# Performance work log

Hardware: AMD Instinct MI355X
Metric: run time of the kernel (lower is better)

## Reference

```python
import jax, jax.numpy as jnp
import numpy as np

L, B, D, N_LAYERS = 2048, 32, 1024, 4


def setup_inputs() -> dict:
    key = jax.random.key(0)
    ks = jax.random.split(key, 5)
    # PyTorch Linear default init: U(-1/sqrt(fan_in), 1/sqrt(fan_in))
    bound = 1.0 / np.sqrt(D)
    x = jax.random.normal(ks[0], (L, B, D), dtype=jnp.float32)
    A_log = jnp.log(0.99) * jnp.ones((D,), dtype=jnp.float32)  # matches torch init
    layers_W = jax.random.uniform(ks[1], (N_LAYERS, D, D), jnp.float32, -bound, bound)
    layers_b = jax.random.uniform(ks[2], (N_LAYERS, D), jnp.float32, -bound, bound)
    head_W = jax.random.uniform(ks[3], (1, D), jnp.float32, -bound, bound)
    head_b = jax.random.uniform(ks[4], (1,), jnp.float32, -bound, bound)
    return {"x": x, "A_log": A_log, "layers_W": layers_W, "layers_b": layers_b,
            "head_W": head_W, "head_b": head_b}


def reference(x, A_log, layers_W, layers_b, head_W, head_b):
    Lx, Bx, Dx = x.shape
    # log_P[t] = (t+1) * A_log  (cumsum of the constant log_A along time)
    log_P = jnp.cumsum(jnp.broadcast_to(A_log[None, None, :], (Lx, Bx, Dx)), axis=0)
    P = jnp.exp(log_P)                       # [L, B, D]
    h = P * jnp.cumsum(x / P, axis=0)        # diagonal linear SSM scan
    for i in range(layers_W.shape[0]):
        h = jnp.tanh(jnp.einsum('lbd,ed->lbe', h, layers_W[i]) + layers_b[i])
    out = jnp.einsum('lbd,ed->lbe', h, head_W) + head_b  # [L, B, 1]
    return out.squeeze(-1)                   # [L, B]
```

## Files before the change

kernel.cpp:

```cpp
#include <hip/hip_runtime.h>
#include <cstdint>
#include <cstddef>

#define LSEQ 2048
#define BB   32
#define DD   1024
#define NLAYERS 4
#define MM   (LSEQ*BB)
#define BD   (BB*DD)
#define CHUNK 32
#define NCHUNK (LSEQ/CHUNK)

typedef _Float16 f16;
typedef __attribute__((ext_vector_type(8))) _Float16 f16x8;
typedef __attribute__((ext_vector_type(4))) float f32x4;


__global__ void scan_pass1(const float* __restrict__ x, const float* __restrict__ Alog,
                           f16* __restrict__ h, float* __restrict__ carry) {
    int tid = blockIdx.x * blockDim.x + threadIdx.x;
    int bd  = tid & (BD - 1);
    int c   = tid >> 15;
    float a = expf(Alog[bd & (DD - 1)]);
    size_t base = (size_t)c * CHUNK * BD + bd;
    float hv = 0.f;
#pragma unroll
    for (int i = 0; i < CHUNK; ++i) {
        hv = a * hv + x[base + (size_t)i * BD];
        h[base + (size_t)i * BD] = (f16)hv;
    }
    carry[c * BD + bd] = hv;
}

__global__ void scan_pass2(const float* __restrict__ Alog, float* __restrict__ carry) {
    int bd = blockIdx.x * blockDim.x + threadIdx.x;
    float d32 = expf((float)CHUNK * Alog[bd & (DD - 1)]);
    float cin = 0.f;
    for (int c = 0; c < NCHUNK; ++c) {
        float co = carry[c * BD + bd];
        carry[c * BD + bd] = cin;
        cin = d32 * cin + co;
    }
}

__global__ void scan_pass3(const float* __restrict__ Alog, const float* __restrict__ carry,
                           f16* __restrict__ h) {
    int tid = blockIdx.x * blockDim.x + threadIdx.x;
    int bd  = tid & (BD - 1);
    int c   = tid >> 15;
    float a   = expf(Alog[bd & (DD - 1)]);
    float cin = carry[c * BD + bd];
    size_t base = (size_t)c * CHUNK * BD + bd;
    float p = a;
#pragma unroll
    for (int i = 0; i < CHUNK; ++i) {
        size_t idx = base + (size_t)i * BD;
        float hv = (float)h[idx] + p * cin;
        h[idx] = (f16)hv;
        p *= a;
    }
}


__global__ void cvt_w(const float* __restrict__ w, f16* __restrict__ o, int n) {
    int i = (blockIdx.x * blockDim.x + threadIdx.x) * 4;
    if (i + 3 < n) {
        float4 v = *(const float4*)&w[i];
        o[i + 0] = (f16)v.x; o[i + 1] = (f16)v.y;
        o[i + 2] = (f16)v.z; o[i + 3] = (f16)v.w;
    }
}


#define BM 256
#define BN 256
#define BK 64
#define KK 1024
#define NN 1024
#define NKTILE (KK / BK)
#define NITER  (NKTILE / 2)

__device__ __forceinline__ void gload_lds16(const void* g, void* l) {
    __builtin_amdgcn_global_load_lds((const __attribute__((address_space(1))) unsigned int*)g,
                                     (__attribute__((address_space(3))) unsigned int*)l,
                                     16, 0, 0);
}

__device__ __forceinline__ void stage_half(const f16* __restrict__ gbase, f16* region, int tid) {
#pragma unroll
    for (int j = 0; j < 2; ++j) {
        int s = tid + j * 512;
        int r = s >> 3;
        int c = (s & 7) ^ (r & 7);
        gload_lds16(gbase + (size_t)r * KK + c * 8, region + (size_t)s * 8);
    }
}

__device__ __forceinline__ void stage_tile(const f16* __restrict__ gA, const f16* __restrict__ gW,
                                           f16* As, f16* Bs, int tid) {
    stage_half(gA,                    As,        tid);
    stage_half(gA + (size_t)128 * KK, As + 8192, tid);
    stage_half(gW,                    Bs,        tid);
    stage_half(gW + (size_t)128 * KK, Bs + 8192, tid);
}

__device__ __forceinline__ f16x8 rd(const f16* base, int row, int chunk) {
    int c = chunk ^ (row & 7);
    return *(const f16x8*)(base + row * 64 + c * 8);
}

__device__ __forceinline__ float tanh_fast(float z) {
    float e = __expf(2.f * z);
    return 1.f - 2.f / (e + 1.f);
}

#define BAR() do { __builtin_amdgcn_sched_barrier(0); __builtin_amdgcn_s_barrier(); \
                   __builtin_amdgcn_sched_barrier(0); } while (0)

__global__ __launch_bounds__(512, 2) void gemm_tanh(const f16* __restrict__ A,
                                                    const f16* __restrict__ W,
                                                    const float* __restrict__ bias,
                                                    f16* __restrict__ C) {
    __shared__ f16 As[2][BM * BK];
    __shared__ f16 Bs[2][BN * BK];

    const int tid  = threadIdx.x;
    const int lane = tid & 63;
    const int wid  = tid >> 6;
    const int wr   = wid >> 2;
    const int wc   = wid & 3;

    const int cpx = gridDim.x >> 3;
    const int lin = ((int)blockIdx.x & 7) * cpx + ((int)blockIdx.x >> 3);
    const int tm  = (lin >> 2) * BM;
    const int tn  = (lin & 3) * BN;

    const f16* Ab = A + (size_t)tm * KK;
    const f16* Wb = W + (size_t)tn * KK;

    const int fr = lane & 15;
    const int fc = lane >> 4;

    f32x4 acc[8][4];
#pragma unroll
    for (int i = 0; i < 8; ++i)
#pragma unroll
        for (int j = 0; j < 4; ++j)
            acc[i][j] = (f32x4){0.f, 0.f, 0.f, 0.f};

    stage_tile(Ab,      Wb,      &As[0][0], &Bs[0][0], tid);
    stage_tile(Ab + 64, Wb + 64, &As[1][0], &Bs[1][0], tid);
    asm volatile("s_waitcnt vmcnt(8)" ::: "memory");
    BAR();

    const int arow = wr * 128 + fr;
    const int brow = wc * 64  + fr;

    for (int it = 0; it < NITER; ++it) {
        const bool pf = (it + 1 < NITER);
        const int kt0 = 2 * it;
        const f16* Ac = &As[0][0]; const f16* Bc = &Bs[0][0];
        const f16* Ad = &As[1][0]; const f16* Bd = &Bs[1][0];
        f16x8 a0[8], b0[4], a1[8], b1[4];

#pragma unroll
        for (int m = 0; m < 8; ++m) a0[m] = rd(Ac, arow + m * 16, fc);
#pragma unroll
        for (int n = 0; n < 4; ++n) b0[n] = rd(Bc, brow + n * 16, fc);
#pragma unroll
        for (int m = 0; m < 8; ++m) a1[m] = rd(Ac, arow + m * 16, 4 + fc);
#pragma unroll
        for (int n = 0; n < 4; ++n) b1[n] = rd(Bc, brow + n * 16, 4 + fc);
        BAR();
        __builtin_amdgcn_s_setprio(1);
#pragma unroll
        for (int m = 0; m < 8; ++m)
#pragma unroll
            for (int n = 0; n < 4; ++n)
                acc[m][n] = __builtin_amdgcn_mfma_f32_16x16x32_f16(a0[m], b0[n], acc[m][n], 0, 0, 0);
        __builtin_amdgcn_s_setprio(0);
        asm volatile("s_waitcnt lgkmcnt(0)" ::: "memory");
        BAR();

        if (pf) stage_tile(Ab + (size_t)(kt0 + 2) * BK, Wb + (size_t)(kt0 + 2) * BK,
                           &As[0][0], &Bs[0][0], tid);
        __builtin_amdgcn_s_setprio(1);
#pragma unroll
        for (int m = 0; m < 8; ++m)
#pragma unroll
            for (int n = 0; n < 4; ++n)
                acc[m][n] = __builtin_amdgcn_mfma_f32_16x16x32_f16(a1[m], b1[n], acc[m][n], 0, 0, 0);
        __builtin_amdgcn_s_setprio(0);
        if (pf) asm volatile("s_waitcnt vmcnt(8)" ::: "memory");
        else    asm volatile("s_waitcnt vmcnt(0)" ::: "memory");
        BAR();

#pragma unroll
        for (int m = 0; m < 8; ++m) a0[m] = rd(Ad, arow + m * 16, fc);
#pragma unroll
        for (int n = 0; n < 4; ++n) b0[n] = rd(Bd, brow + n * 16, fc);
#pragma unroll
        for (int m = 0; m < 8; ++m) a1[m] = rd(Ad, arow + m * 16, 4 + fc);
#pragma unroll
        for (int n = 0; n < 4; ++n) b1[n] = rd(Bd, brow + n * 16, 4 + fc);
        BAR();
        __builtin_amdgcn_s_setprio(1);
#pragma unroll
        for (int m = 0; m < 8; ++m)
#pragma unroll
            for (int n = 0; n < 4; ++n)
                acc[m][n] = __builtin_amdgcn_mfma_f32_16x16x32_f16(a0[m], b0[n], acc[m][n], 0, 0, 0);
        __builtin_amdgcn_s_setprio(0);
        asm volatile("s_waitcnt lgkmcnt(0)" ::: "memory");
        BAR();

        if (pf) stage_tile(Ab + (size_t)(kt0 + 3) * BK, Wb + (size_t)(kt0 + 3) * BK,
                           &As[1][0], &Bs[1][0], tid);
        __builtin_amdgcn_s_setprio(1);
#pragma unroll
        for (int m = 0; m < 8; ++m)
#pragma unroll
            for (int n = 0; n < 4; ++n)
                acc[m][n] = __builtin_amdgcn_mfma_f32_16x16x32_f16(a1[m], b1[n], acc[m][n], 0, 0, 0);
        __builtin_amdgcn_s_setprio(0);
        if (pf) asm volatile("s_waitcnt vmcnt(8)" ::: "memory");
        else    asm volatile("s_waitcnt vmcnt(0)" ::: "memory");
        BAR();
    }

#pragma unroll
    for (int mi = 0; mi < 8; ++mi) {
        const int r0 = tm + wr * 128 + mi * 16 + (fc << 2);
#pragma unroll
        for (int ni = 0; ni < 4; ++ni) {
            const int c = tn + wc * 64 + ni * 16 + fr;
            const float bv = bias[c];
#pragma unroll
            for (int q = 0; q < 4; ++q) {
                float z = acc[mi][ni][q] + bv;
                C[(size_t)(r0 + q) * NN + c] = (f16)tanh_fast(z);
            }
        }
    }
}


__global__ void head_k(const f16* __restrict__ h, const float* __restrict__ hw,
                       const float* __restrict__ hb, float* __restrict__ out) {
    const int row  = blockIdx.x * 4 + (threadIdx.x >> 6);
    const int lane = threadIdx.x & 63;
    const f16* hr = h + (size_t)row * DD;
    float s = 0.f;
#pragma unroll
    for (int j = 0; j < DD / 64; ++j) {
        int d = lane + j * 64;
        s += (float)hr[d] * hw[d];
    }
#pragma unroll
    for (int o = 32; o > 0; o >>= 1) s += __shfl_down(s, o, 64);
    if (lane == 0) out[row] = s + hb[0];
}


extern "C" void kernel_launch(void* const* d_in, const int* in_sizes, int n_in,
                              void* d_out, int out_size, void* d_ws, size_t ws_size,
                              hipStream_t stream) {
    const float* x    = (const float*)d_in[0];
    const float* Alog = (const float*)d_in[1];
    const float* Wls  = (const float*)d_in[2];
    const float* bls  = (const float*)d_in[3];
    const float* hw   = (const float*)d_in[4];
    const float* hb   = (const float*)d_in[5];
    float* out = (float*)d_out;

    char* ws = (char*)d_ws;
    const size_t hbytes = (size_t)MM * DD * sizeof(f16);
    f16* h0 = (f16*)ws;
    f16* h1 = (f16*)(ws + hbytes);
    char* scratch = ws + 2 * hbytes;
    float* carry = (float*)scratch;
    f16*   wf    = (f16*)scratch;

    scan_pass1<<<(NCHUNK * BD) / 256, 256, 0, stream>>>(x, Alog, h0, carry);
    scan_pass2<<<BD / 256, 256, 0, stream>>>(Alog, carry);
    scan_pass3<<<(NCHUNK * BD) / 256, 256, 0, stream>>>(Alog, carry, h0);

    cvt_w<<<(NLAYERS * DD * DD / 4) / 256, 256, 0, stream>>>(Wls, wf, NLAYERS * DD * DD);

    dim3 grid((MM / BM) * (NN / BN)), blk(512);
    gemm_tanh<<<grid, blk, 0, stream>>>(h0, wf + 0 * (DD * DD), bls + 0 * DD, h1);
    gemm_tanh<<<grid, blk, 0, stream>>>(h1, wf + 1 * (DD * DD), bls + 1 * DD, h0);
    gemm_tanh<<<grid, blk, 0, stream>>>(h0, wf + 2 * (DD * DD), bls + 2 * DD, h1);
    gemm_tanh<<<grid, blk, 0, stream>>>(h1, wf + 3 * (DD * DD), bls + 3 * DD, h0);

    head_k<<<MM / 4, 256, 0, stream>>>(h0, hw, hb, out);
}
```

Before: 781.3 us.

## Software-pipeline LDS fragment reads with MFMA in GEMM main loop

Restructures the GEMM k-loop so the LDS fragment reads for the next half-tile are issued before the MFMA block on the current fragments, overlapping LDS latency with matrix math. The global-to-LDS staging and its waits now happen between barriers without MFMAs in flight, and the first fragment read is hoisted out of the loop. This removes the idle time where MFMAs waited on LDS reads. It adds live registers for the double fragment sets and changes barrier placement, which could affect occupancy or correctness of buffer reuse.

```diff
diff --git a/kernel.cpp b/kernel.cpp
--- a/kernel.cpp
+++ b/kernel.cpp
@@ -78,7 +78,6 @@
 #define KK 1024
 #define NN 1024
 #define NKTILE (KK / BK)
-#define NITER  (NKTILE / 2)
 
 __device__ __forceinline__ void gload_lds16(const void* g, void* l) {
     __builtin_amdgcn_global_load_lds((const __attribute__((address_space(1))) unsigned int*)g,
@@ -109,6 +108,15 @@
     return *(const f16x8*)(base + row * 64 + c * 8);
 }
 
+__device__ __forceinline__ void read12(const f16* Abase, const f16* Bbase,
+                                       int arow, int brow, int kc,
+                                       f16x8 a[8], f16x8 b[4]) {
+#pragma unroll
+    for (int m = 0; m < 8; ++m) a[m] = rd(Abase, arow + m * 16, kc);
+#pragma unroll
+    for (int n = 0; n < 4; ++n) b[n] = rd(Bbase, brow + n * 16, kc);
+}
+
 __device__ __forceinline__ float tanh_fast(float z) {
     float e = __expf(2.f * z);
     return 1.f - 2.f / (e + 1.f);
@@ -116,6 +124,17 @@
 
 #define BAR() do { __builtin_amdgcn_sched_barrier(0); __builtin_amdgcn_s_barrier(); \
                    __builtin_amdgcn_sched_barrier(0); } while (0)
+
+#define MFMA32(av, bv) do {                                                     \
+    __builtin_amdgcn_s_setprio(1);                                              \
+    _Pragma("unroll")                                                           \
+    for (int m = 0; m < 8; ++m)                                                 \
+        _Pragma("unroll")                                                       \
+        for (int n = 0; n < 4; ++n)                                             \
+            acc[m][n] = __builtin_amdgcn_mfma_f32_16x16x32_f16(av[m], bv[n],    \
+                                                               acc[m][n], 0, 0, 0); \
+    __builtin_amdgcn_s_setprio(0);                                              \
+} while (0)
 
 __global__ __launch_bounds__(512, 2) void gemm_tanh(const f16* __restrict__ A,
                                                     const f16* __restrict__ W,
@@ -156,76 +175,43 @@
     const int arow = wr * 128 + fr;
     const int brow = wc * 64  + fr;
 
-    for (int it = 0; it < NITER; ++it) {
-        const bool pf = (it + 1 < NITER);
-        const int kt0 = 2 * it;
-        const f16* Ac = &As[0][0]; const f16* Bc = &Bs[0][0];
-        const f16* Ad = &As[1][0]; const f16* Bd = &Bs[1][0];
-        f16x8 a0[8], b0[4], a1[8], b1[4];
-
-#pragma unroll
-        for (int m = 0; m < 8; ++m) a0[m] = rd(Ac, arow + m * 16, fc);
-#pragma unroll
-        for (int n = 0; n < 4; ++n) b0[n] = rd(Bc, brow + n * 16, fc);
-#pragma unroll
-        for (int m = 0; m < 8; ++m) a1[m] = rd(Ac, arow + m * 16, 4 + fc);
-#pragma unroll
-        for (int n = 0; n < 4; ++n) b1[n] = rd(Bc, brow + n * 16, 4 + fc);
-        BAR();
-        __builtin_amdgcn_s_setprio(1);
-#pragma unroll
-        for (int m = 0; m < 8; ++m)
-#pragma unroll
-            for (int n = 0; n < 4; ++n)
-                acc[m][n] = __builtin_amdgcn_mfma_f32_16x16x32_f16(a0[m], b0[n], acc[m][n], 0, 0, 0);
-        __builtin_amdgcn_s_setprio(0);
+    f16x8 a0[8], b0[4], a1[8], b1[4];
+    read12(&As[0][0], &Bs[0][0], arow, brow, fc, a0, b0);
+
+    for (int it = 0; it < NKTILE / 2; ++it) {
+        const bool pf = (it + 1 < NKTILE / 2);
+
+        read12(&As[0][0], &Bs[0][0], arow, brow, 4 + fc, a1, b1);
+        __builtin_amdgcn_sched_barrier(0);
+        MFMA32(a0, b0);
         asm volatile("s_waitcnt lgkmcnt(0)" ::: "memory");
         BAR();
-
-        if (pf) stage_tile(Ab + (size_t)(kt0 + 2) * BK, Wb + (size_t)(kt0 + 2) * BK,
-                           &As[0][0], &Bs[0][0], tid);
-        __builtin_amdgcn_s_setprio(1);
-#pragma unroll
-        for (int m = 0; m < 8; ++m)
-#pragma unroll
-            for (int n = 0; n < 4; ++n)
-                acc[m][n] = __builtin_amdgcn_mfma_f32_16x16x32_f16(a1[m], b1[n], acc[m][n], 0, 0, 0);
-        __builtin_amdgcn_s_setprio(0);
-        if (pf) asm volatile("s_waitcnt vmcnt(8)" ::: "memory");
-        else    asm volatile("s_waitcnt vmcnt(0)" ::: "memory");
-        BAR();
-
-#pragma unroll
-        for (int m = 0; m < 8; ++m) a0[m] = rd(Ad, arow + m * 16, fc);
-#pragma unroll
-        for (int n = 0; n < 4; ++n) b0[n] = rd(Bd, brow + n * 16, fc);
-#pragma unroll
-        for (int m = 0; m < 8; ++m) a1[m] = rd(Ad, arow + m * 16, 4 + fc);
-#pragma unroll
-        for (int n = 0; n < 4; ++n) b1[n] = rd(Bd, brow + n * 16, 4 + fc);
-        BAR();
-        __builtin_amdgcn_s_setprio(1);
-#pragma unroll
-        for (int m = 0; m < 8; ++m)
-#pragma unroll
-            for (int n = 0; n < 4; ++n)
-                acc[m][n] = __builtin_amdgcn_mfma_f32_16x16x32_f16(a0[m], b0[n], acc[m][n], 0, 0, 0);
-        __builtin_amdgcn_s_setprio(0);
+        if (pf) {
+            stage_tile(Ab + (size_t)(2 * it + 2) * BK, Wb + (size_t)(2 * it + 2) * BK,
+                       &As[0][0], &Bs[0][0], tid);
+            asm volatile("s_waitcnt vmcnt(8)" ::: "memory");
+        } else {
+            asm volatile("s_waitcnt vmcnt(0)" ::: "memory");
+        }
+        BAR();
+        read12(&As[1][0], &Bs[1][0], arow, brow, fc, a0, b0);
+        __builtin_amdgcn_sched_barrier(0);
+        MFMA32(a1, b1);
+
+        read12(&As[1][0], &Bs[1][0], arow, brow, 4 + fc, a1, b1);
+        __builtin_amdgcn_sched_barrier(0);
+        MFMA32(a0, b0);
         asm volatile("s_waitcnt lgkmcnt(0)" ::: "memory");
         BAR();
-
-        if (pf) stage_tile(Ab + (size_t)(kt0 + 3) * BK, Wb + (size_t)(kt0 + 3) * BK,
-                           &As[1][0], &Bs[1][0], tid);
-        __builtin_amdgcn_s_setprio(1);
-#pragma unroll
-        for (int m = 0; m < 8; ++m)
-#pragma unroll
-            for (int n = 0; n < 4; ++n)
-                acc[m][n] = __builtin_amdgcn_mfma_f32_16x16x32_f16(a1[m], b1[n], acc[m][n], 0, 0, 0);
-        __builtin_amdgcn_s_setprio(0);
-        if (pf) asm volatile("s_waitcnt vmcnt(8)" ::: "memory");
-        else    asm volatile("s_waitcnt vmcnt(0)" ::: "memory");
-        BAR();
+        if (pf) {
+            stage_tile(Ab + (size_t)(2 * it + 3) * BK, Wb + (size_t)(2 * it + 3) * BK,
+                       &As[1][0], &Bs[1][0], tid);
+            asm volatile("s_waitcnt vmcnt(8)" ::: "memory");
+        }
+        BAR();
+        if (pf) read12(&As[0][0], &Bs[0][0], arow, brow, fc, a0, b0);
+        __builtin_amdgcn_sched_barrier(0);
+        MFMA32(a1, b1);
     }
 
 #pragma unroll
```

Measured after the change: 922.3 us. 1.18x slower.
